# Kernel optimization log

Hardware: AMD Instinct MI355X
Metric: run time of the kernel (lower is better)

Reference implementation:

```python
import jax, jax.numpy as jnp
import numpy as np

THR = 1.0   # snntorch Leaky default threshold
BETA = 0.9  # leak factor from the module


@jax.custom_vjp
def atan_spike(x):
    # Heaviside forward; ATan surrogate gradient (snntorch default alpha=2):
    # d/dx = 1 / (1 + (pi * x)^2)
    return (x > 0).astype(x.dtype)

def _atan_fwd(x):
    return (x > 0).astype(x.dtype), x

def _atan_bwd(x, g):
    return (g / (1.0 + (jnp.pi * x) ** 2),)

atan_spike.defvjp(_atan_fwd, _atan_bwd)


def setup_inputs() -> dict:
    key = jax.random.key(0)
    k0, k1, k2, k3, k4 = jax.random.split(key, 5)
    B, T, L = 256, 1000, 30  # 24 = L - 7 + 1 matches fc1 in_features 16*24
    out_c = 35
    x = jax.random.normal(k0, (B, T, L), dtype=jnp.float32)
    conv_w = jax.random.normal(k1, (16, 1, 7), dtype=jnp.float32) / np.float32(np.sqrt(7.0))
    conv_b = jax.random.normal(k2, (16,), dtype=jnp.float32) * 0.05
    fc_w = jax.random.normal(k3, (out_c, 16 * 24), dtype=jnp.float32) / np.float32(np.sqrt(384.0))
    fc_b = jax.random.normal(k4, (out_c,), dtype=jnp.float32) * 0.05
    return {"x": x, "conv_w": conv_w, "conv_b": conv_b, "fc_w": fc_w, "fc_b": fc_b}


def reference(x, conv_w, conv_b, fc_w, fc_b):
    B, T, L = x.shape
    # Conv1d has no recurrence -> hoist it out of the time loop, batched over B*T.
    cur1 = jax.lax.conv_general_dilated(
        x.reshape(B * T, 1, L), conv_w, window_strides=(1,), padding="VALID",
        dimension_numbers=("NCH", "OIH", "NCH"),
    ) + conv_b[None, :, None]                      # (B*T, 16, 24)
    Lo = cur1.shape[-1]
    cur1 = cur1.reshape(B, T, 16, Lo).transpose(1, 0, 2, 3)  # (T, B, 16, 24)
    out_c = fc_w.shape[0]

    def step(carry, c1):
        mem1, mem2 = carry
        # LIF1: reset-by-subtraction using detached spike of previous membrane
        r1 = jax.lax.stop_gradient((mem1 > THR).astype(mem1.dtype))
        mem1 = BETA * mem1 + c1 - r1 * THR
        spk1 = atan_spike(mem1 - THR)              # (B, 16, 24)
        c2 = spk1.reshape(B, 16 * Lo) @ fc_w.T + fc_b  # (B, out_c)
        # LIF2
        r2 = jax.lax.stop_gradient((mem2 > THR).astype(mem2.dtype))
        mem2 = BETA * mem2 + c2 - r2 * THR
        return (mem1, mem2), mem2

    init = (jnp.zeros((B, 16, Lo), x.dtype), jnp.zeros((B, out_c), x.dtype))
    _, mem2_rec = jax.lax.scan(step, init, cur1)   # (T, B, out_c)
    return mem2_rec.mean(axis=0)                   # (B, out_c)
```

## Files before the change

kernel.cpp:

```cpp
#include <hip/hip_runtime.h>

typedef _Float16 half8 __attribute__((ext_vector_type(8)));
typedef float f32x4 __attribute__((ext_vector_type(4)));

#define SPH  32
#define SPKW 392
#define XTW  36
#define C2W  48
#define TN   1000


#define LOADBLK(BUF, S)                                                 \
    _Pragma("unroll")                                                   \
    for (int k = 0; k < 7; ++k)                                         \
        BUF[k] = *(const f32x4*)(xcol + k * XTW + (S));

#define CONV4(BUF, SB)                                                  \
    {                                                                   \
        float ca[4], cc[4];                                             \
        _Pragma("unroll")                                               \
        for (int dt = 0; dt < 4; ++dt) { ca[dt] = cb0; cc[dt] = cb1; }  \
        _Pragma("unroll")                                               \
        for (int k = 0; k < 7; ++k) {                                   \
            _Pragma("unroll")                                           \
            for (int dt = 0; dt < 4; ++dt) {                            \
                ca[dt] = fmaf(wk0[k], BUF[k][dt], ca[dt]);              \
                cc[dt] = fmaf(wk1[k], BUF[k][dt], cc[dt]);              \
            }                                                           \
        }                                                               \
        _Pragma("unroll")                                               \
        for (int dt = 0; dt < 4; ++dt) {                                \
            m1a = fmaf(0.9f, m1a, ca[dt] - spa);                        \
            spa = (m1a > 1.0f) ? 1.0f : 0.0f;                           \
            m1b = fmaf(0.9f, m1b, cc[dt] - spb);                        \
            spb = (m1b > 1.0f) ? 1.0f : 0.0f;                           \
            unsigned int pk = (m1a > 1.0f ? 0x00003C00u : 0u) |         \
                              (m1b > 1.0f ? 0x3C000000u : 0u);          \
            sdst[((SB) + dt) * (SPKW / 2)] = pk;                        \
        }                                                               \
    }

__global__ __launch_bounds__(576, 1) void snn_fwd(
    const float* __restrict__ x,
    const float* __restrict__ conv_w,
    const float* __restrict__ conv_b,
    const float* __restrict__ fc_w,
    const float* __restrict__ fc_b,
    float* __restrict__ out)
{
    __shared__ __align__(16) _Float16 spk[2][SPH][SPKW];
    __shared__ __align__(16) float    xsT[2][30][XTW];
    __shared__ __align__(16) float    c2L[2][SPH][C2W];

    const int tid  = threadIdx.x;
    const int b    = blockIdx.x >> 1;
    const int half = blockIdx.x & 1;
    const int wid  = tid >> 6;
    const int lane = tid & 63;

    const int D0      = half ? 15 : 0;
    const int CONV_HI = half ? 31 : 16;
    const int acc_lo  = half ? 544 : 0;
    const int acc_hi  = half ? TN : 544;

    const int ct    = tid;
    const int cpair = ct & 7;
    const int p     = ct >> 3;
    const int c0    = cpair * 2;
    float wk0[7], wk1[7];
    float cb0 = 0.f, cb1 = 0.f;
    if (wid < 3) {
#pragma unroll
        for (int k = 0; k < 7; ++k) {
            wk0[k] = conv_w[c0 * 7 + k];
            wk1[k] = conv_w[(c0 + 1) * 7 + k];
        }
        cb0 = conv_b[c0];
        cb1 = conv_b[c0 + 1];
    }

    const int g  = wid - 3;
    const int m  = g >> 1;
    const int tb = g & 1;
    const int nL = lane & 15;
    const int q  = lane >> 4;
    half8 A[12];
    if (wid >= 3) {
        const int o = m * 16 + nL;
#pragma unroll
        for (int kt = 0; kt < 12; ++kt) {
            half8 a;
#pragma unroll
            for (int j = 0; j < 8; ++j) {
                int Kp = kt * 32 + q * 8 + j;
                int Kc = Kp & 15;
                int Kq = Kp >> 4;
                a[j] = (o < 35) ? (_Float16)fc_w[o * 384 + Kc * 24 + Kq]
                                : (_Float16)0.f;
            }
            A[kt] = a;
        }
    }
    const float fcb = (wid == 3 && lane < 35) ? fc_b[lane] : 0.f;

    const int st = tid - 192;
    int fs[3], fl[3];
    if (wid >= 3) {
#pragma unroll
        for (int r = 0; r < 3; ++r) {
            int f = st + 384 * r;
            fs[r] = f / 30;
            fl[r] = f % 30;
        }
    }

    float m1a = 0.f, spa = 0.f;
    float m1b = 0.f, spb = 0.f;
    float mem2 = 0.f, accO = 0.f;
    float xr[3];

    const float* xb = x + (size_t)b * (TN * 30);

    if (wid >= 3) {
        const float* xpro = xb + (size_t)D0 * (SPH * 30);
#pragma unroll
        for (int r = 0; r < 3; ++r) {
            int f = st + 384 * r;
            if (f < 960) xsT[D0 & 1][fl[r]][fs[r]] = xpro[f];
        }
#pragma unroll
        for (int r = 0; r < 3; ++r) {
            int f = st + 384 * r;
            xr[r] = (f < 960) ? xpro[960 + f] : 0.f;
        }
    }
    __syncthreads();

#pragma unroll 1
    for (int ph = 0; ph < 19; ++ph) {
        const int d = D0 + ph;
        if (wid < 3) {
            if (d <= CONV_HI) {
                const float* xcol = &xsT[d & 1][p][0];
                unsigned int* sdst =
                    (unsigned int*)&spk[d & 1][0][p * 16 + c0];

                f32x4 bufA[7], bufB[7];
                LOADBLK(bufA, 0)
#pragma unroll
                for (int blk = 0; blk < 8; blk += 2) {
                    LOADBLK(bufB, (blk + 1) * 4)
                    CONV4(bufA, blk * 4)
                    if (blk + 2 < 8) { LOADBLK(bufA, (blk + 2) * 4) }
                    CONV4(bufB, (blk + 1) * 4)
                }
            }
        } else {
            const bool ldg = (d + 2 <= CONV_HI);
            float xn[3];
            if (ldg) {
                const float* src = xb + (size_t)(d + 2) * (SPH * 30);
#pragma unroll
                for (int r = 0; r < 3; ++r) {
                    int f = st + 384 * r;
                    int t = (d + 2) * SPH + fs[r];
                    xn[r] = (f < 960 && t < TN) ? src[f] : 0.f;
                }
            }
            if (ph >= 1 && d - 1 <= CONV_HI) {
                const _Float16* sb = &spk[(d - 1) & 1][0][0];
                half8 B[12];
#pragma unroll
                for (int kt = 0; kt < 12; ++kt)
                    B[kt] = *(const half8*)(sb + (tb * 16 + nL) * SPKW + kt * 32 + q * 8);
                f32x4 acc = {0.f, 0.f, 0.f, 0.f};
#pragma unroll
                for (int kt = 0; kt < 12; ++kt)
                    acc = __builtin_amdgcn_mfma_f32_16x16x32_f16(A[kt], B[kt], acc, 0, 0, 0);
                float* cd = &c2L[(d - 1) & 1][0][0];
                *(f32x4*)(cd + (tb * 16 + nL) * C2W + m * 16 + q * 4) = acc;
            }
            if (wid == 3 && lane < 35 && ph >= 2 && d - 2 <= CONV_HI) {
                const float* cs = &c2L[(d - 2) & 1][0][0];
                float v[SPH];
#pragma unroll
                for (int j = 0; j < SPH; ++j) v[j] = cs[j * C2W + lane];
                const int tbase = (d - 2) * SPH;
#pragma unroll
                for (int j = 0; j < SPH; ++j) {
                    float r2 = (mem2 > 1.0f) ? 1.0f : 0.0f;
                    mem2 = 0.9f * mem2 + (v[j] + fcb) - r2;
                    int t = tbase + j;
                    if (t >= acc_lo && t < acc_hi) accO += mem2;
                }
            }
            if (d + 1 <= CONV_HI) {
                float* dst = &xsT[(d + 1) & 1][0][0];
#pragma unroll
                for (int r = 0; r < 3; ++r) {
                    int f = st + 384 * r;
                    if (f < 960) dst[fl[r] * XTW + fs[r]] = xr[r];
                }
            }
            if (ldg) {
#pragma unroll
                for (int r = 0; r < 3; ++r) xr[r] = xn[r];
            }
        }
        __syncthreads();
    }

    if (wid == 3 && lane < 35)
        atomicAdd(&out[b * 35 + lane], accO * (1.0f / (float)TN));
}

extern "C" void kernel_launch(void* const* d_in, const int* in_sizes, int n_in,
                              void* d_out, int out_size, void* d_ws, size_t ws_size,
                              hipStream_t stream) {
    const float* x      = (const float*)d_in[0];
    const float* conv_w = (const float*)d_in[1];
    const float* conv_b = (const float*)d_in[2];
    const float* fc_w   = (const float*)d_in[3];
    const float* fc_b   = (const float*)d_in[4];
    float* out          = (float*)d_out;

    snn_fwd<<<512, 576, 0, stream>>>(x, conv_w, conv_b, fc_w, fc_b, out);
}
```

Measured before the change: 167.5 us.

## Shrink block to 8 waves, each MFMA wave covers both time tiles

The block shrinks from 9 to 8 waves. Three MFMA waves each loop over both 16-step time tiles instead of six waves handling one tile each, and the LIF2 recurrence moves to a dedicated wave 6. The x-staging stride changes so 320 threads cover the 960 elements exactly, which removes the bounds predicates. This cuts block size and wave overhead, but each MFMA wave now does twice the serial work per phase, which could lengthen the critical path.

Result: faster. 163.9 us (-2.1%).

```diff
diff --git a/kernel.cpp b/kernel.cpp
--- a/kernel.cpp
+++ b/kernel.cpp
@@ -40,7 +40,7 @@
         }                                                               \
     }
 
-__global__ __launch_bounds__(576, 1) void snn_fwd(
+__global__ __launch_bounds__(512, 1) void snn_fwd(
     const float* __restrict__ x,
     const float* __restrict__ conv_w,
     const float* __restrict__ conv_b,
@@ -79,13 +79,11 @@
         cb1 = conv_b[c0 + 1];
     }
 
-    const int g  = wid - 3;
-    const int m  = g >> 1;
-    const int tb = g & 1;
+    const int m  = wid - 3;
     const int nL = lane & 15;
     const int q  = lane >> 4;
     half8 A[12];
-    if (wid >= 3) {
+    if (wid >= 3 && wid < 6) {
         const int o = m * 16 + nL;
 #pragma unroll
         for (int kt = 0; kt < 12; ++kt) {
@@ -101,14 +99,14 @@
             A[kt] = a;
         }
     }
-    const float fcb = (wid == 3 && lane < 35) ? fc_b[lane] : 0.f;
+    const float fcb = (wid == 6 && lane < 35) ? fc_b[lane] : 0.f;
 
     const int st = tid - 192;
     int fs[3], fl[3];
     if (wid >= 3) {
 #pragma unroll
         for (int r = 0; r < 3; ++r) {
-            int f = st + 384 * r;
+            int f = st + 320 * r;
             fs[r] = f / 30;
             fl[r] = f % 30;
         }
@@ -124,15 +122,11 @@
     if (wid >= 3) {
         const float* xpro = xb + (size_t)D0 * (SPH * 30);
 #pragma unroll
-        for (int r = 0; r < 3; ++r) {
-            int f = st + 384 * r;
-            if (f < 960) xsT[D0 & 1][fl[r]][fs[r]] = xpro[f];
-        }
-#pragma unroll
-        for (int r = 0; r < 3; ++r) {
-            int f = st + 384 * r;
-            xr[r] = (f < 960) ? xpro[960 + f] : 0.f;
-        }
+        for (int r = 0; r < 3; ++r)
+            xsT[D0 & 1][fl[r]][fs[r]] = xpro[st + 320 * r];
+#pragma unroll
+        for (int r = 0; r < 3; ++r)
+            xr[r] = xpro[960 + st + 320 * r];
     }
     __syncthreads();
 
@@ -162,25 +156,27 @@
                 const float* src = xb + (size_t)(d + 2) * (SPH * 30);
 #pragma unroll
                 for (int r = 0; r < 3; ++r) {
-                    int f = st + 384 * r;
                     int t = (d + 2) * SPH + fs[r];
-                    xn[r] = (f < 960 && t < TN) ? src[f] : 0.f;
-                }
-            }
-            if (ph >= 1 && d - 1 <= CONV_HI) {
+                    xn[r] = (t < TN) ? src[st + 320 * r] : 0.f;
+                }
+            }
+            if (wid < 6 && ph >= 1 && d - 1 <= CONV_HI) {
                 const _Float16* sb = &spk[(d - 1) & 1][0][0];
-                half8 B[12];
-#pragma unroll
-                for (int kt = 0; kt < 12; ++kt)
-                    B[kt] = *(const half8*)(sb + (tb * 16 + nL) * SPKW + kt * 32 + q * 8);
-                f32x4 acc = {0.f, 0.f, 0.f, 0.f};
-#pragma unroll
-                for (int kt = 0; kt < 12; ++kt)
-                    acc = __builtin_amdgcn_mfma_f32_16x16x32_f16(A[kt], B[kt], acc, 0, 0, 0);
                 float* cd = &c2L[(d - 1) & 1][0][0];
-                *(f32x4*)(cd + (tb * 16 + nL) * C2W + m * 16 + q * 4) = acc;
-            }
-            if (wid == 3 && lane < 35 && ph >= 2 && d - 2 <= CONV_HI) {
+#pragma unroll
+                for (int tb = 0; tb < 2; ++tb) {
+                    half8 B[12];
+#pragma unroll
+                    for (int kt = 0; kt < 12; ++kt)
+                        B[kt] = *(const half8*)(sb + (tb * 16 + nL) * SPKW + kt * 32 + q * 8);
+                    f32x4 acc = {0.f, 0.f, 0.f, 0.f};
+#pragma unroll
+                    for (int kt = 0; kt < 12; ++kt)
+                        acc = __builtin_amdgcn_mfma_f32_16x16x32_f16(A[kt], B[kt], acc, 0, 0, 0);
+                    *(f32x4*)(cd + (tb * 16 + nL) * C2W + m * 16 + q * 4) = acc;
+                }
+            }
+            if (wid == 6 && lane < 35 && ph >= 2 && d - 2 <= CONV_HI) {
                 const float* cs = &c2L[(d - 2) & 1][0][0];
                 float v[SPH];
 #pragma unroll
@@ -197,10 +193,8 @@
             if (d + 1 <= CONV_HI) {
                 float* dst = &xsT[(d + 1) & 1][0][0];
 #pragma unroll
-                for (int r = 0; r < 3; ++r) {
-                    int f = st + 384 * r;
-                    if (f < 960) dst[fl[r] * XTW + fs[r]] = xr[r];
-                }
+                for (int r = 0; r < 3; ++r)
+                    dst[fl[r] * XTW + fs[r]] = xr[r];
             }
             if (ldg) {
 #pragma unroll
@@ -210,7 +204,7 @@
         __syncthreads();
     }
 
-    if (wid == 3 && lane < 35)
+    if (wid == 6 && lane < 35)
         atomicAdd(&out[b * 35 + lane], accO * (1.0f / (float)TN));
 }
 
@@ -224,5 +218,5 @@
     const float* fc_b   = (const float*)d_in[4];
     float* out          = (float*)d_out;
 
-    snn_fwd<<<512, 576, 0, stream>>>(x, conv_w, conv_b, fc_w, fc_b, out);
+    snn_fwd<<<512, 512, 0, stream>>>(x, conv_w, conv_b, fc_w, fc_b, out);
 }
```
